# Performance work log

Hardware: AMD Instinct MI355X
Metric: run time of the kernel (lower is better)

The kernel has to match this reference:

```python
import jax, jax.numpy as jnp
import numpy as np

N_NODES = 30000
N_REL = 8
N_EDGES = 131072
IN_FEAT = 512
OUT_FEAT = 512


def setup_inputs() -> dict:
    key = jax.random.key(0)
    k1, k2, k3, k4, k5 = jax.random.split(key, 5)
    x = jax.random.normal(k1, (N_NODES, IN_FEAT), dtype=jnp.float32)
    # per-relation weights [R, in, out] (xavier-ish scale)
    weight = jax.random.normal(k2, (N_REL, IN_FEAT, OUT_FEAT), dtype=jnp.float32) * (2.0 / (IN_FEAT + OUT_FEAT)) ** 0.5
    loop_weight = jax.random.normal(k3, (IN_FEAT, OUT_FEAT), dtype=jnp.float32) * (2.0 / (IN_FEAT + OUT_FEAT)) ** 0.5
    h_bias = jnp.zeros((OUT_FEAT,), dtype=jnp.float32)
    src = jax.random.randint(k4, (N_REL, N_EDGES), 0, N_NODES, dtype=jnp.int32)
    dst = jax.random.randint(k5, (N_REL, N_EDGES), 0, N_NODES, dtype=jnp.int32)
    return {"x": x, "weight": weight, "loop_weight": loop_weight,
            "h_bias": h_bias, "src": src, "dst": dst}


def reference(x, weight, loop_weight, h_bias, src, dst):
    # Per-relation GraphConv(norm='right', weight=W_r):
    #   transform all node feats, gather on src, scatter-sum on dst,
    #   normalize by in-degree (clamped to 1). Relations summed (HeteroGraphConv 'sum').
    xw = jnp.einsum('ni,rio->rno', x, weight)  # [R, N, out]

    def per_rel(xw_r, src_r, dst_r):
        msgs = xw_r[src_r]  # [E, out] gathered messages
        agg = jax.ops.segment_sum(msgs, dst_r, num_segments=N_NODES)
        deg = jax.ops.segment_sum(jnp.ones_like(dst_r, dtype=xw_r.dtype), dst_r,
                                  num_segments=N_NODES)
        return agg / jnp.clip(deg, 1.0)[:, None]

    h = jax.vmap(per_rel)(xw, src, dst).sum(axis=0)  # [N, out]
    h = h + x @ loop_weight + h_bias  # self-loop + bias
    return jax.nn.relu(h)  # activation; dropout=0.0 -> identity
```

## Files before the change

kernel.cpp:

```cpp
#include <hip/hip_runtime.h>
#include <hip/hip_bf16.h>

#define N_NODES 30000
#define N_REL   8
#define N_EDGES 131072
#define FEAT    512
#define KTOT    4608
#define CAP     32

typedef __attribute__((ext_vector_type(8))) __bf16 v8bf;
typedef __attribute__((ext_vector_type(4))) __bf16 v4bf;
typedef __attribute__((ext_vector_type(4))) float  v4f;
typedef __attribute__((ext_vector_type(2))) float  f2;
typedef __attribute__((ext_vector_type(8))) unsigned short u16x8;

static __device__ __forceinline__ void load_lds16(const void* g, void* l) {
  __builtin_amdgcn_global_load_lds(
      (const __attribute__((address_space(1))) void*)g,
      (__attribute__((address_space(3))) void*)l, 16, 0, 0);
}

#define CONV_BLOCKS 15000
#define TR_BLOCKS   2304
#define CNT_BLOCKS  512
__global__ __launch_bounds__(256)
void k_prep(const float* __restrict__ x, const float* __restrict__ w,
            const float* __restrict__ lw, const int* __restrict__ src,
            const int* __restrict__ dst, __bf16* __restrict__ xbf,
            __bf16* __restrict__ Wt, int* __restrict__ cnt,
            unsigned short* __restrict__ slots) {
  __shared__ float t[32][33];
  const int b = blockIdx.x, tid = threadIdx.x;
  if (b < CONV_BLOCKS) {
    int i = b * 256 + tid;
    float4 v = ((const float4*)x)[i];
    v4bf o;
    o[0] = (__bf16)v.x; o[1] = (__bf16)v.y; o[2] = (__bf16)v.z; o[3] = (__bf16)v.w;
    ((v4bf*)xbf)[i] = o;
  } else if (b < CONV_BLOCKS + TR_BLOCKS) {
    int tb = b - CONV_BLOCKS;
    int k0 = (tb % 144) * 32, n0 = (tb / 144) * 32;
    int tx = tid & 31, ty = tid >> 5;
    #pragma unroll
    for (int q = 0; q < 4; ++q) {
      int k = k0 + ty + q * 8, n = n0 + tx;
      float v = (k < 4096) ? w[(size_t)k * 512 + n] : lw[(size_t)(k - 4096) * 512 + n];
      t[ty + q * 8][tx] = v;
    }
    __syncthreads();
    #pragma unroll
    for (int q = 0; q < 4; ++q) {
      int n = n0 + ty + q * 8, k = k0 + tx;
      Wt[(size_t)n * KTOT + k] = (__bf16)t[tx][ty + q * 8];
    }
  } else {
    int cb  = b - CONV_BLOCKS - TR_BLOCKS;
    int rel = cb & 7;
    int q   = cb >> 3;
    int e0  = rel * N_EDGES + (q * 256 + tid) * 8;
    int4 sa = *(const int4*)(src + e0), sb = *(const int4*)(src + e0 + 4);
    int4 da = *(const int4*)(dst + e0), db = *(const int4*)(dst + e0 + 4);
    int ss[8] = {sa.x, sa.y, sa.z, sa.w, sb.x, sb.y, sb.z, sb.w};
    int dd[8] = {da.x, da.y, da.z, da.w, db.x, db.y, db.z, db.w};
    int bb[8], pp[8];
    #pragma unroll
    for (int j = 0; j < 8; ++j) {
      bb[j] = rel * N_NODES + dd[j];
      pp[j] = atomicAdd(&cnt[bb[j]], 1);
    }
    #pragma unroll
    for (int j = 0; j < 8; ++j)
      if (pp[j] < CAP) slots[(size_t)bb[j] * CAP + pp[j]] = (unsigned short)ss[j];
  }
}

__global__ __launch_bounds__(256)
void k_aggregate(const __bf16* __restrict__ xbf, const int* __restrict__ cnt,
                 const unsigned short* __restrict__ slots,
                 __bf16* __restrict__ out, int nBuckets) {
  int w = (blockIdx.x * blockDim.x + threadIdx.x) >> 6;
  int lane = threadIdx.x & 63;
  if (w >= nBuckets) return;
  const unsigned short* sl = slots + (size_t)w * CAP;
  u16x8 qs[4];
  qs[0] = *(const u16x8*)(sl);
  qs[1] = *(const u16x8*)(sl + 8);
  qs[2] = *(const u16x8*)(sl + 16);
  qs[3] = *(const u16x8*)(sl + 24);
  int c = cnt[w];
  int cc = c < CAP ? c : CAP;
  const __bf16* xb = xbf + (size_t)lane * 8;
  f2 acc2[4];
  #pragma unroll
  for (int p = 0; p < 4; ++p) acc2[p] = (f2){0.f, 0.f};
  #pragma unroll
  for (int g = 0; g < 4; ++g) {
    if (cc > g * 8) {
      int m = cc - g * 8;
      v8bf r[8];
      #pragma unroll
      for (int j = 0; j < 8; ++j)
        if (m > j) r[j] = *(const v8bf*)(xb + (size_t)qs[g][j] * FEAT);
      #pragma unroll
      for (int j = 0; j < 8; ++j)
        if (m > j) {
          const unsigned* ru = (const unsigned*)&r[j];
          #pragma unroll
          for (int p = 0; p < 4; ++p) {
            f2 v;
            v[0] = __uint_as_float(ru[p] << 16);
            v[1] = __uint_as_float(ru[p] & 0xffff0000u);
            acc2[p] += v;
          }
        }
    }
  }
  float scale = 1.0f / (float)(c > 1 ? c : 1);
  v8bf o;
  #pragma unroll
  for (int p = 0; p < 4; ++p) {
    o[2 * p]     = (__bf16)(acc2[p][0] * scale);
    o[2 * p + 1] = (__bf16)(acc2[p][1] * scale);
  }
  *(v8bf*)(out + (size_t)w * FEAT + lane * 8) = o;
}

template <bool ACCUM, bool FINAL>
__global__ __launch_bounds__(512, 2)
void k_gemm3(const __bf16* __restrict__ A, size_t slabStride,
             const __bf16* __restrict__ Wt, int kTiles,
             const float* __restrict__ bias, float* __restrict__ C) {
  __shared__ __align__(16) char smem[131072];

  const int tid  = threadIdx.x;
  const int wave = tid >> 6, lane = tid & 63;
  const int lr = lane >> 3, lc = lane & 7;
  const int gcs = (lc ^ lr) * 8;
  const int quad = lane >> 4, l15 = lane & 15;
  const int wR2 = wave >> 2;
  const int wC4 = wave & 3;

  const int nwg = gridDim.x;
  const int qq = nwg >> 3, rr = nwg & 7;
  const int xcd = blockIdx.x & 7, oidx = blockIdx.x >> 3;
  const int wg = (xcd < rr ? xcd * (qq + 1) : rr * (qq + 1) + (xcd - rr) * qq) + oidx;
  const int mtile = wg >> 1, ntile = wg & 1;
  const int mBase = mtile * 256, nBase = ntile * 256;

  v4f acc[2][2][4][2];
  #pragma unroll
  for (int a = 0; a < 2; ++a)
    #pragma unroll
    for (int bq = 0; bq < 2; ++bq)
      #pragma unroll
      for (int mi = 0; mi < 4; ++mi)
        #pragma unroll
        for (int ni = 0; ni < 2; ++ni)
          acc[a][bq][mi][ni] = (v4f){0.f, 0.f, 0.f, 0.f};

  auto stageA = [&](int t, int h) {
    __bf16* dst = (__bf16*)(smem + (t & 1) * 65536);
    const int kk = t * 64;
    const __bf16* base = A + (size_t)(kk >> 9) * slabStride + (kk & 511);
    #pragma unroll
    for (int r2 = 0; r2 < 2; ++r2) {
      int rt = h * 128 + r2 * 64 + wave * 8;
      int row = mBase + rt + lr;
      if (row > N_NODES - 1) row = N_NODES - 1;
      load_lds16(base + (size_t)row * FEAT + gcs, dst + rt * 64);
    }
  };
  auto stageB = [&](int t, int h) {
    __bf16* dst = (__bf16*)(smem + (t & 1) * 65536 + 32768);
    const int kk = t * 64;
    #pragma unroll
    for (int r2 = 0; r2 < 2; ++r2) {
      int rt = h * 128 + r2 * 64 + wave * 8;
      int n = nBase + rt + lr;
      load_lds16(Wt + (size_t)n * KTOT + kk + gcs, dst + rt * 64);
    }
  };

  stageA(0, 0); stageB(0, 0); stageB(0, 1); stageA(0, 1);
  asm volatile("s_waitcnt vmcnt(4)" ::: "memory");
  __builtin_amdgcn_s_barrier();
  __builtin_amdgcn_sched_barrier(0);

  for (int t = 0; t < kTiles; ++t) {
    const __bf16* sA = (const __bf16*)(smem + (t & 1) * 65536);
    const __bf16* sB = sA + 16384;
    const bool pf = (t + 1) < kTiles;
    v8bf af[4][2], bf0[2][2], bf1[2][2];

    #pragma unroll
    for (int mi = 0; mi < 4; ++mi)
      #pragma unroll
      for (int ks = 0; ks < 2; ++ks) {
        int m = wR2 * 64 + mi * 16 + l15;
        int q = ks * 4 + quad;
        af[mi][ks] = *(const v8bf*)(sA + m * 64 + ((q ^ (m & 7)) * 8));
      }
    #pragma unroll
    for (int ni = 0; ni < 2; ++ni)
      #pragma unroll
      for (int ks = 0; ks < 2; ++ks) {
        int n = wC4 * 32 + ni * 16 + l15;
        int q = ks * 4 + quad;
        bf0[ni][ks] = *(const v8bf*)(sB + n * 64 + ((q ^ (n & 7)) * 8));
      }
    if (pf) stageA(t + 1, 0);
    __builtin_amdgcn_s_barrier();
    asm volatile("s_waitcnt lgkmcnt(0)" ::: "memory");
    __builtin_amdgcn_sched_barrier(0);
    __builtin_amdgcn_s_setprio(1);
    #pragma unroll
    for (int ks = 0; ks < 2; ++ks)
      #pragma unroll
      for (int mi = 0; mi < 4; ++mi)
        #pragma unroll
        for (int ni = 0; ni < 2; ++ni)
          acc[0][0][mi][ni] = __builtin_amdgcn_mfma_f32_16x16x32_bf16(
              af[mi][ks], bf0[ni][ks], acc[0][0][mi][ni], 0, 0, 0);
    __builtin_amdgcn_s_setprio(0);
    if (pf) asm volatile("s_waitcnt vmcnt(4)" ::: "memory");
    else    asm volatile("s_waitcnt vmcnt(2)" ::: "memory");
    __builtin_amdgcn_s_barrier();
    __builtin_amdgcn_sched_barrier(0);

    #pragma unroll
    for (int ni = 0; ni < 2; ++ni)
      #pragma unroll
      for (int ks = 0; ks < 2; ++ks) {
        int n = 128 + wC4 * 32 + ni * 16 + l15;
        int q = ks * 4 + quad;
        bf1[ni][ks] = *(const v8bf*)(sB + n * 64 + ((q ^ (n & 7)) * 8));
      }
    if (pf) stageB(t + 1, 0);
    __builtin_amdgcn_s_barrier();
    asm volatile("s_waitcnt lgkmcnt(0)" ::: "memory");
    __builtin_amdgcn_sched_barrier(0);
    __builtin_amdgcn_s_setprio(1);
    #pragma unroll
    for (int ks = 0; ks < 2; ++ks)
      #pragma unroll
      for (int mi = 0; mi < 4; ++mi)
        #pragma unroll
        for (int ni = 0; ni < 2; ++ni)
          acc[0][1][mi][ni] = __builtin_amdgcn_mfma_f32_16x16x32_bf16(
              af[mi][ks], bf1[ni][ks], acc[0][1][mi][ni], 0, 0, 0);
    __builtin_amdgcn_s_setprio(0);
    if (pf) asm volatile("s_waitcnt vmcnt(4)" ::: "memory");
    else    asm volatile("s_waitcnt vmcnt(0)" ::: "memory");
    __builtin_amdgcn_s_barrier();
    __builtin_amdgcn_sched_barrier(0);

    #pragma unroll
    for (int mi = 0; mi < 4; ++mi)
      #pragma unroll
      for (int ks = 0; ks < 2; ++ks) {
        int m = 128 + wR2 * 64 + mi * 16 + l15;
        int q = ks * 4 + quad;
        af[mi][ks] = *(const v8bf*)(sA + m * 64 + ((q ^ (m & 7)) * 8));
      }
    if (pf) stageB(t + 1, 1);
    __builtin_amdgcn_s_barrier();
    asm volatile("s_waitcnt lgkmcnt(0)" ::: "memory");
    __builtin_amdgcn_sched_barrier(0);
    __builtin_amdgcn_s_setprio(1);
    #pragma unroll
    for (int ks = 0; ks < 2; ++ks)
      #pragma unroll
      for (int mi = 0; mi < 4; ++mi)
        #pragma unroll
        for (int ni = 0; ni < 2; ++ni)
          acc[1][1][mi][ni] = __builtin_amdgcn_mfma_f32_16x16x32_bf16(
              af[mi][ks], bf1[ni][ks], acc[1][1][mi][ni], 0, 0, 0);
    __builtin_amdgcn_s_setprio(0);
    __builtin_amdgcn_s_barrier();
    __builtin_amdgcn_sched_barrier(0);

    if (pf) stageA(t + 1, 1);
    __builtin_amdgcn_s_barrier();
    __builtin_amdgcn_s_setprio(1);
    #pragma unroll
    for (int ks = 0; ks < 2; ++ks)
      #pragma unroll
      for (int mi = 0; mi < 4; ++mi)
        #pragma unroll
        for (int ni = 0; ni < 2; ++ni)
          acc[1][0][mi][ni] = __builtin_amdgcn_mfma_f32_16x16x32_bf16(
              af[mi][ks], bf0[ni][ks], acc[1][0][mi][ni], 0, 0, 0);
    __builtin_amdgcn_s_setprio(0);
    if (pf) asm volatile("s_waitcnt vmcnt(4)" ::: "memory");
    __builtin_amdgcn_s_barrier();
    __builtin_amdgcn_sched_barrier(0);
  }

  asm volatile("s_waitcnt vmcnt(0)" ::: "memory");
  float* cbuf = (float*)smem;
  const int f4 = tid & 63;
  const int colg = nBase + f4 * 4;
  v4f bias4 = (v4f){0.f, 0.f, 0.f, 0.f};
  if (FINAL) bias4 = *(const v4f*)(bias + colg);
  #pragma unroll
  for (int h = 0; h < 4; ++h) {
    __syncthreads();
    if (wR2 == (h & 1)) {
      const int R = h >> 1;
      #pragma unroll
      for (int Cq = 0; Cq < 2; ++Cq)
        #pragma unroll
        for (int mi = 0; mi < 4; ++mi)
          #pragma unroll
          for (int ni = 0; ni < 2; ++ni)
            #pragma unroll
            for (int e = 0; e < 4; ++e)
              cbuf[(mi * 16 + quad * 4 + e) * 260 + Cq * 128 + wC4 * 32 + ni * 16 + l15] =
                  acc[R][Cq][mi][ni][e];
    }
    __syncthreads();
    #pragma unroll
    for (int i = 0; i < 8; ++i) {
      int rl  = i * 8 + (tid >> 6);
      int row = mBase + h * 64 + rl;
      if (row < N_NODES) {
        v4f v = *(const v4f*)(cbuf + rl * 260 + f4 * 4);
        size_t idx = (size_t)row * FEAT + colg;
        if (ACCUM) v += *(const v4f*)(C + idx);
        if (FINAL) {
          #pragma unroll
          for (int e = 0; e < 4; ++e) v[e] = fmaxf(v[e] + bias4[e], 0.f);
        }
        *(v4f*)(C + idx) = v;
      }
    }
  }
}

template <bool ACCUM, bool FINAL>
__global__ __launch_bounds__(256, 4)
void k_gemm(const __bf16* __restrict__ A, size_t slabStride,
            const __bf16* __restrict__ Wt, int wtStride, int kTiles,
            const float* __restrict__ bias, float* __restrict__ C,
            int mtBase, int mtEnd) {
  __shared__ __align__(16) char smem[33792];
  __bf16* As = (__bf16*)smem;
  __bf16* Bs = (__bf16*)(smem + 16384);

  const int tid  = threadIdx.x;
  const int wave = tid >> 6;
  const int lane = tid & 63;
  const int lr = lane >> 3, lc = lane & 7;
  const int gcs = (lc ^ lr) * 8;
  const int quad = lane >> 4, l15 = lane & 15;
  const int wRow = wave >> 1, wCol = wave & 1;

  const int panel = blockIdx.x >> 5;
  const int w32   = blockIdx.x & 31;
  const int mtile = mtBase + panel * 8 + (w32 & 7);
  const int ntile = w32 >> 3;
  if (mtile >= mtEnd) return;
  const int mBase = mtile * 128;
  const int nBase = ntile * 128;

  v4f acc[4][4];
  #pragma unroll
  for (int i = 0; i < 4; ++i)
    #pragma unroll
    for (int j = 0; j < 4; ++j) acc[i][j] = (v4f){0.f, 0.f, 0.f, 0.f};

  for (int kt = 0; kt < kTiles; ++kt) {
    const int kk = kt * 64;
    const __bf16* aT = A + (size_t)(kk >> 9) * slabStride + (kk & 511);
    #pragma unroll
    for (int t = 0; t < 4; ++t) {
      int chunk = wave * 4 + t;
      int row = mBase + chunk * 8 + lr;
      if (row > N_NODES - 1) row = N_NODES - 1;
      load_lds16(aT + (size_t)row * FEAT + gcs, As + chunk * 512);
      int n = nBase + chunk * 8 + lr;
      load_lds16(Wt + (size_t)n * wtStride + kk + gcs, Bs + chunk * 512);
    }
    __syncthreads();
    #pragma unroll
    for (int ks = 0; ks < 2; ++ks) {
      const int q = ks * 4 + quad;
      v8bf af[4], bfr[4];
      #pragma unroll
      for (int mi = 0; mi < 4; ++mi) {
        int m = wRow * 64 + mi * 16 + l15;
        af[mi] = *(const v8bf*)(As + m * 64 + ((q ^ (m & 7)) * 8));
      }
      #pragma unroll
      for (int ni = 0; ni < 4; ++ni) {
        int n = wCol * 64 + ni * 16 + l15;
        bfr[ni] = *(const v8bf*)(Bs + n * 64 + ((q ^ (n & 7)) * 8));
      }
      #pragma unroll
      for (int mi = 0; mi < 4; ++mi)
        #pragma unroll
        for (int ni = 0; ni < 4; ++ni)
          acc[mi][ni] = __builtin_amdgcn_mfma_f32_16x16x32_bf16(af[mi], bfr[ni], acc[mi][ni], 0, 0, 0);
    }
    __syncthreads();
  }

  float* cbuf = (float*)smem;
  const int f4c  = tid & 31;
  const int colg = nBase + f4c * 4;
  v4f bias4 = (v4f){0.f, 0.f, 0.f, 0.f};
  if (FINAL) bias4 = *(const v4f*)(bias + colg);
  #pragma unroll
  for (int h = 0; h < 2; ++h) {
    if (wRow == h) {
      #pragma unroll
      for (int mi = 0; mi < 4; ++mi) {
        int r0 = mi * 16 + quad * 4;
        #pragma unroll
        for (int ni = 0; ni < 4; ++ni) {
          int c = wCol * 64 + ni * 16 + l15;
          #pragma unroll
          for (int e = 0; e < 4; ++e)
            cbuf[(r0 + e) * 132 + c] = acc[mi][ni][e];
        }
      }
    }
    __syncthreads();
    #pragma unroll
    for (int i = 0; i < 8; ++i) {
      int rh  = (tid >> 5) + 8 * i;
      int row = mBase + h * 64 + rh;
      if (row < N_NODES) {
        v4f v = *(const v4f*)(cbuf + rh * 132 + f4c * 4);
        size_t idx = (size_t)row * FEAT + colg;
        if (ACCUM) v += *(const v4f*)(C + idx);
        if (FINAL) {
          #pragma unroll
          for (int e = 0; e < 4; ++e) v[e] = fmaxf(v[e] + bias4[e], 0.f);
        }
        *(v4f*)(C + idx) = v;
      }
    }
    __syncthreads();
  }
}

extern "C" void kernel_launch(void* const* d_in, const int* in_sizes, int n_in,
                              void* d_out, int out_size, void* d_ws, size_t ws_size,
                              hipStream_t stream) {
  const float* x    = (const float*)d_in[0];
  const float* w    = (const float*)d_in[1];
  const float* lw   = (const float*)d_in[2];
  const float* bias = (const float*)d_in[3];
  const int*   src  = (const int*)d_in[4];
  const int*   dst  = (const int*)d_in[5];
  float* out = (float*)d_out;

  char* ws = (char*)d_ws;
  const size_t SLAB  = (size_t)N_NODES * FEAT;
  const size_t slabB = SLAB * 2;
  const size_t wtB   = (size_t)FEAT * KTOT * 2;
  const size_t cntB  = (size_t)N_REL * N_NODES * 4;
  const size_t slotB = (size_t)N_REL * N_NODES * CAP * 2;
  const size_t fixedB = wtB + cntB + slotB;

  __bf16*         Wt     = (__bf16*)ws;
  int*            cnt    = (int*)(ws + wtB);
  unsigned short* slots  = (unsigned short*)(ws + wtB + cntB);
  __bf16*         slabs  = (__bf16*)(ws + fixedB);

  int nSlab = (int)((ws_size - fixedB) / slabB);
  int g = nSlab - 1;
  if (g > 7) g = 7;
  if (g < 1) g = 1;
  __bf16* xbf = slabs + (size_t)g * SLAB;

  hipMemsetAsync(cnt, 0, cntB, stream);
  k_prep<<<CONV_BLOCKS + TR_BLOCKS + CNT_BLOCKS, 256, 0, stream>>>(
      x, w, lw, src, dst, xbf, Wt, cnt, slots);

  if (g == 7) {
    const int mt256 = (N_NODES + 255) / 256;
    const int grid3 = mt256 * 2;
    k_aggregate<<<(7 * N_NODES) / 4, 256, 0, stream>>>(xbf, cnt, slots,
                                                       slabs, 7 * N_NODES);
    k_gemm3<false, false><<<grid3, 512, 0, stream>>>(
        slabs, SLAB, Wt, 3584 / 64, bias, out);
    k_aggregate<<<N_NODES / 4, 256, 0, stream>>>(
        xbf, cnt + 7 * N_NODES, slots + (size_t)7 * N_NODES * CAP,
        slabs + (size_t)6 * SLAB, N_NODES);
    k_gemm3<true, true><<<grid3, 512, 0, stream>>>(
        slabs + (size_t)6 * SLAB, SLAB, Wt + 3584, 1024 / 64, bias, out);
  } else {
    const int nMtiles = (N_NODES + 127) / 128;
    const int gemmGrid = ((nMtiles + 7) / 8) * 32;
    for (int r0 = 0; r0 < N_REL; r0 += g) {
      int gc2 = (N_REL - r0) < g ? (N_REL - r0) : g;
      k_aggregate<<<(gc2 * N_NODES) / 4, 256, 0, stream>>>(
          xbf, cnt + r0 * N_NODES, slots + (size_t)r0 * N_NODES * CAP,
          slabs, gc2 * N_NODES);
      if (r0 == 0)
        k_gemm<false, false><<<gemmGrid, 256, 0, stream>>>(
            slabs, SLAB, Wt + r0 * 512, KTOT, gc2 * 8, bias, out, 0, nMtiles);
      else
        k_gemm<true, false><<<gemmGrid, 256, 0, stream>>>(
            slabs, SLAB, Wt + r0 * 512, KTOT, gc2 * 8, bias, out, 0, nMtiles);
    }
    k_gemm<true, true><<<gemmGrid, 256, 0, stream>>>(xbf, SLAB, Wt + 4096, KTOT,
                                                     8, bias, out, 0, nMtiles);
  }
}
```

Before: 527.7 us.

## Slice aggregation gather by feature columns to improve cache locality

Adds a sliced aggregation kernel where each block processes one 64-column slice of the feature dimension for 32 destination buckets, with grid order slice-major. All blocks working on a slice gather from the same narrow strip of the node feature matrix, which is meant to fit in cache and cut random DRAM traffic from the edge gather. In exchange, slot lists and counts are re-read once per slice, and each gathered fragment is only 16 bytes per row.

```diff
diff --git a/kernel.cpp b/kernel.cpp
--- a/kernel.cpp
+++ b/kernel.cpp
@@ -75,6 +75,74 @@
 }
 
 __global__ __launch_bounds__(256)
+void k_agg_slice(const __bf16* __restrict__ xbf, const int* __restrict__ cnt,
+                 const unsigned short* __restrict__ slots,
+                 __bf16* __restrict__ out, int nBuckets, int bps) {
+  const int bid   = blockIdx.x;
+  const int slice = bid / bps;
+  const int ib    = bid - slice * bps;
+  const int tid   = threadIdx.x;
+  const int wave  = tid >> 6, lane = tid & 63;
+  const int grp   = lane >> 3;
+  const int li    = lane & 7;
+  const int w     = ib * 32 + wave * 8 + grp;
+  const bool valid = (w < nBuckets);
+
+  int c = 0;
+  u16x8 qs[4];
+  if (valid) {
+    c = cnt[w];
+    const unsigned short* sl = slots + (size_t)w * CAP;
+    qs[0] = *(const u16x8*)(sl);
+    qs[1] = *(const u16x8*)(sl + 8);
+    qs[2] = *(const u16x8*)(sl + 16);
+    qs[3] = *(const u16x8*)(sl + 24);
+  }
+  int cc = c < CAP ? c : CAP;
+  int cmax = cc;
+  cmax = max(cmax, __shfl_xor(cmax, 8));
+  cmax = max(cmax, __shfl_xor(cmax, 16));
+  cmax = max(cmax, __shfl_xor(cmax, 32));
+
+  const __bf16* xb = xbf + slice * 64 + (size_t)li * 8;
+  f2 acc2[4];
+  #pragma unroll
+  for (int p = 0; p < 4; ++p) acc2[p] = (f2){0.f, 0.f};
+  #pragma unroll
+  for (int g = 0; g < 4; ++g) {
+    if (cmax > g * 8) {
+      v8bf r[8];
+      #pragma unroll
+      for (int j = 0; j < 8; ++j)
+        if (cc > g * 8 + j)
+          r[j] = *(const v8bf*)(xb + (size_t)qs[g][j] * FEAT);
+      #pragma unroll
+      for (int j = 0; j < 8; ++j)
+        if (cc > g * 8 + j) {
+          const unsigned* ru = (const unsigned*)&r[j];
+          #pragma unroll
+          for (int p = 0; p < 4; ++p) {
+            f2 v;
+            v[0] = __uint_as_float(ru[p] << 16);
+            v[1] = __uint_as_float(ru[p] & 0xffff0000u);
+            acc2[p] += v;
+          }
+        }
+    }
+  }
+  if (valid) {
+    float scale = 1.0f / (float)(c > 1 ? c : 1);
+    v8bf o;
+    #pragma unroll
+    for (int p = 0; p < 4; ++p) {
+      o[2 * p]     = (__bf16)(acc2[p][0] * scale);
+      o[2 * p + 1] = (__bf16)(acc2[p][1] * scale);
+    }
+    *(v8bf*)(out + (size_t)w * FEAT + slice * 64 + (size_t)li * 8) = o;
+  }
+}
+
+__global__ __launch_bounds__(256)
 void k_aggregate(const __bf16* __restrict__ xbf, const int* __restrict__ cnt,
                  const unsigned short* __restrict__ slots,
                  __bf16* __restrict__ out, int nBuckets) {
@@ -482,13 +550,15 @@
   if (g == 7) {
     const int mt256 = (N_NODES + 255) / 256;
     const int grid3 = mt256 * 2;
-    k_aggregate<<<(7 * N_NODES) / 4, 256, 0, stream>>>(xbf, cnt, slots,
-                                                       slabs, 7 * N_NODES);
+    const int bps1 = (7 * N_NODES + 31) / 32;
+    k_agg_slice<<<8 * bps1, 256, 0, stream>>>(xbf, cnt, slots,
+                                              slabs, 7 * N_NODES, bps1);
     k_gemm3<false, false><<<grid3, 512, 0, stream>>>(
         slabs, SLAB, Wt, 3584 / 64, bias, out);
-    k_aggregate<<<N_NODES / 4, 256, 0, stream>>>(
+    const int bps2 = (N_NODES + 31) / 32;
+    k_agg_slice<<<8 * bps2, 256, 0, stream>>>(
         xbf, cnt + 7 * N_NODES, slots + (size_t)7 * N_NODES * CAP,
-        slabs + (size_t)6 * SLAB, N_NODES);
+        slabs + (size_t)6 * SLAB, N_NODES, bps2);
     k_gemm3<true, true><<<grid3, 512, 0, stream>>>(
         slabs + (size_t)6 * SLAB, SLAB, Wt + 3584, 1024 / 64, bias, out);
   } else {
```

Measured after the change: 499.1 us. -5.4%, faster.
